# Kernel tuning notes

Measured on AMD Instinct MI355X. Metric: run time of the kernel, lower is better.

The kernel has to match this reference:

```python
import jax, jax.numpy as jnp
import numpy as np


def setup_inputs() -> dict:
    key = jax.random.key(0)
    ks = jax.random.split(key, 8)
    dim, E = 128, 8
    b, t, h, w = 2, 16, 64, 64
    scale = 1.0 / np.sqrt(dim)
    return {
        "x": jax.random.normal(ks[0], (b, dim, t, h, w), jnp.float32),
        "gate_w": jax.random.normal(ks[1], (dim, E), jnp.float32) * scale,
        "gate_b": jax.random.normal(ks[2], (E,), jnp.float32) * 0.01,
        "W1": jax.random.normal(ks[3], (E, dim, dim), jnp.float32) * scale,
        "b1": jax.random.normal(ks[4], (E, dim), jnp.float32) * 0.01,
        "alpha": jnp.full((E,), 0.25, jnp.float32),  # PReLU default init
        "W2": jax.random.normal(ks[5], (E, dim, dim), jnp.float32) * scale,
        "b2": jax.random.normal(ks[6], (E, dim), jnp.float32) * 0.01,
        "top_k": 2,
    }


def reference(x, gate_w, gate_b, W1, b1, alpha, W2, b2, top_k):
    b, c, t, h, w = x.shape
    E = gate_w.shape[1]
    # tokens: [N, c] with N = b*t*h*w (matches permute(0,2,3,4,1).reshape(-1,c))
    xf = jnp.transpose(x, (0, 2, 3, 4, 1)).reshape(-1, c)
    N = xf.shape[0]
    logits = xf @ gate_w + gate_b                      # [N, E]
    vals, idx = jax.lax.top_k(logits, top_k)           # [N, K]
    probs = jax.nn.softmax(vals, axis=1)               # softmax over selected logits
    # scatter combine weights to dense [N, E] (zero for unselected experts)
    combine = jnp.zeros((N, E), xf.dtype).at[jnp.arange(N)[:, None], idx].add(probs)
    # expert MLP (1x1x1 conv == per-token linear), scalar PReLU per expert
    h1 = jnp.einsum('nc,eoc->eno', xf, W1) + b1[:, None, :]          # [E, N, c]
    h1 = jnp.maximum(h1, 0) + alpha[:, None, None] * jnp.minimum(h1, 0)
    h2 = jnp.einsum('eno,epo->enp', h1, W2) + b2[:, None, :]         # [E, N, c]
    out = jnp.einsum('ne,enc->nc', combine, h2)                      # weighted combine
    out = jnp.transpose(out.reshape(b, t, h, w, c), (0, 4, 1, 2, 3))
    return out + x
```

## Files before the change

kernel.cpp:

```cpp
#include <hip/hip_runtime.h>

typedef float f32x4  __attribute__((ext_vector_type(4)));
typedef float f32x16 __attribute__((ext_vector_type(16)));
typedef __bf16 bf16x8 __attribute__((ext_vector_type(8)));

#define SPAT 65536
#define CH   128
#define NE   8

#define SLOTA   0
#define SLOTB   32768
#define GW_OFF  65536
#define B1_OFF  69632
#define B2T_OFF 73728
#define AL_OFF  77824
#define LDS_BYTES 77856

static __device__ __forceinline__ unsigned short f2b(float f) {
    unsigned u = __builtin_bit_cast(unsigned, f);
    unsigned r = u + 0x7FFFu + ((u >> 16) & 1u);
    return (unsigned short)(r >> 16);
}
static __device__ __forceinline__ unsigned pk2(float a, float b) {
    return (unsigned)f2b(a) | ((unsigned)f2b(b) << 16);
}

typedef const __attribute__((address_space(1))) void* as1cp;
typedef __attribute__((address_space(3))) void* as3p;
static __device__ __forceinline__ void gload16(const void* g, void* l) {
    __builtin_amdgcn_global_load_lds((as1cp)g, (as3p)l, 16, 0, 0);
}

__global__ void conv_w(const float* __restrict__ W1, const float* __restrict__ W2,
                       unsigned char* __restrict__ wimg) {
    const int gid = blockIdx.x * 256 + threadIdx.x;
    const int mat = gid >> 14;
    const int e   = (gid >> 11) & 7;
    const int r   = (gid >> 4) & 127;
    const int p   = gid & 15;
    const int sg  = p ^ (r & 15);
    int src_row = r;
    if (mat == 0) {
        const int n = 4 * (r >> 5) + ((r >> 3) & 3);
        src_row = (n >> 1) * 16 + ((r >> 2) & 1) * 8 + (n & 1) * 4 + (r & 3);
    }
    const float* s = (mat ? W2 : W1) + (e * 16384 + src_row * 128 + sg * 8);
    uint4 pk;
    pk.x = pk2(s[0], s[1]); pk.y = pk2(s[2], s[3]);
    pk.z = pk2(s[4], s[5]); pk.w = pk2(s[6], s[7]);
    *(uint4*)(wimg + mat * 262144 + e * 32768 + r * 256 + p * 16) = pk;
}

static __device__ __forceinline__ void stage_w(const unsigned char* __restrict__ src,
                                               unsigned char* dst, int t) {
    const int off = t * 16;
    gload16(src + off,          dst + off);
    gload16(src + 8192  + off,  dst + 8192  + off);
    gload16(src + 16384 + off,  dst + 16384 + off);
    gload16(src + 24576 + off,  dst + 24576 + off);
}

__global__ __launch_bounds__(512, 2)
void moe_main(const float* __restrict__ x,  const float* __restrict__ gw,
              const float* __restrict__ gb, const float* __restrict__ b1,
              const float* __restrict__ alpha, const float* __restrict__ b2,
              const unsigned char* __restrict__ wimg, float* __restrict__ out)
{
    __shared__ __align__(16) unsigned char smem[LDS_BYTES];
    const int t = threadIdx.x, lane = t & 63, w = t >> 6, blk = blockIdx.x;
    const int ltok = lane & 31, hi = lane >> 5, l15 = lane & 15;
    const size_t xbase = (size_t)(blk >> 8) * (size_t)(CH * SPAT) + (size_t)((blk & 255) << 8);
    const int m = w * 32 + ltok;

    stage_w(wimg,          smem + SLOTA, t);
    stage_w(wimg + 262144, smem + SLOTB, t);

    float v[8][8];
    #pragma unroll
    for (int kc = 0; kc < 8; ++kc)
        #pragma unroll
        for (int j = 0; j < 8; ++j)
            v[kc][j] = x[xbase + (size_t)(kc * 16 + hi * 8 + j) * SPAT + m];

    if (t < 256)      ((f32x4*)(smem + GW_OFF))[t]       = ((const f32x4*)gw)[t];
    else              ((f32x4*)(smem + B1_OFF))[t - 256] = ((const f32x4*)b1)[t - 256];
    if (t < 128) {
        uint4 pkv, z4 = {0u, 0u, 0u, 0u};
        pkv.x = pk2(b2[0 * 128 + t], b2[1 * 128 + t]);
        pkv.y = pk2(b2[2 * 128 + t], b2[3 * 128 + t]);
        pkv.z = pk2(b2[4 * 128 + t], b2[5 * 128 + t]);
        pkv.w = pk2(b2[6 * 128 + t], b2[7 * 128 + t]);
        *(uint4*)(smem + B2T_OFF + t * 32)      = pkv;
        *(uint4*)(smem + B2T_OFF + t * 32 + 16) = z4;
    } else if (t >= 128 && t < 136) {
        ((float*)(smem + AL_OFF))[t - 128] = alpha[t - 128];
    }
    __syncthreads();

    f32x4 plo = {0.f,0.f,0.f,0.f}, phi = {0.f,0.f,0.f,0.f};
    uint4 xb[8];
    #pragma unroll
    for (int kc = 0; kc < 8; ++kc) {
        const int c0 = kc * 16 + hi * 8;
        #pragma unroll
        for (int j = 0; j < 8; ++j) {
            const f32x4 g0 = *(const f32x4*)(smem + GW_OFF + (c0 + j) * 32);
            const f32x4 g1 = *(const f32x4*)(smem + GW_OFF + (c0 + j) * 32 + 16);
            plo += v[kc][j] * g0; phi += v[kc][j] * g1;
        }
        xb[kc].x = pk2(v[kc][0], v[kc][1]); xb[kc].y = pk2(v[kc][2], v[kc][3]);
        xb[kc].z = pk2(v[kc][4], v[kc][5]); xb[kc].w = pk2(v[kc][6], v[kc][7]);
    }
    #pragma unroll
    for (int i2 = 0; i2 < 4; ++i2) {
        plo[i2] += __shfl_xor(plo[i2], 32, 64);
        phi[i2] += __shfl_xor(phi[i2], 32, 64);
    }
    int i0, i1; float q0, q1; uint4 cbw;
    {
        float lg[8];
        #pragma unroll
        for (int e2 = 0; e2 < 4; ++e2) { lg[e2] = plo[e2] + gb[e2]; lg[4 + e2] = phi[e2] + gb[4 + e2]; }
        i0 = 0; float v0 = lg[0];
        #pragma unroll
        for (int e2 = 1; e2 < 8; ++e2) if (lg[e2] > v0) { v0 = lg[e2]; i0 = e2; }
        i1 = -1; float v1 = -3.4e38f;
        #pragma unroll
        for (int e2 = 0; e2 < 8; ++e2) if (e2 != i0 && lg[e2] > v1) { v1 = lg[e2]; i1 = e2; }
        const float d = expf(v1 - v0);
        q0 = 1.f / (1.f + d);
        q1 = d   / (1.f + d);
        float cb[8];
        #pragma unroll
        for (int e2 = 0; e2 < 8; ++e2) cb[e2] = (e2 == i0) ? q0 : ((e2 == i1) ? q1 : 0.f);
        cbw.x = pk2(cb[0], cb[1]); cbw.y = pk2(cb[2], cb[3]);
        cbw.z = pk2(cb[4], cb[5]); cbw.w = pk2(cb[6], cb[7]);
    }

    f32x16 acc[4] = {};

    #pragma unroll 1
    for (int e = 0; e < NE; ++e) {
        const float alph = ((const float*)(smem + AL_OFF))[e];
        const float ce = (i0 == e) ? q0 : ((i1 == e) ? q1 : 0.f);

        uint4 pa[8];
        #pragma unroll 2
        for (int g = 0; g < 4; ++g) {
            uint4 a1[8];
            #pragma unroll
            for (int kc = 0; kc < 8; ++kc)
                a1[kc] = *(const uint4*)(smem + SLOTA + (g * 32 + ltok) * 256
                                          + (((kc * 2 + hi) ^ l15) * 16));
            f32x16 h = {};
            #pragma unroll
            for (int kc = 0; kc < 8; ++kc)
                h = __builtin_amdgcn_mfma_f32_32x32x16_bf16(
                        __builtin_bit_cast(bf16x8, a1[kc]),
                        __builtin_bit_cast(bf16x8, xb[kc]), h, 0, 0, 0);
            #pragma unroll
            for (int q = 0; q < 4; ++q) {
                const int n = 4 * g + q, kt2 = n >> 1, half = q & 1;
                const int obase = kt2 * 16 + hi * 8 + half * 4;
                const f32x4 b1v = *(const f32x4*)(smem + B1_OFF + e * 512 + obase * 4);
                float hv[4];
                #pragma unroll
                for (int i = 0; i < 4; ++i) {
                    float z = h[q * 4 + i] + b1v[i];
                    z = (z > 0.f) ? z : alph * z;
                    hv[i] = z * ce;
                }
                ((unsigned*)&pa[kt2])[half * 2]     = pk2(hv[0], hv[1]);
                ((unsigned*)&pa[kt2])[half * 2 + 1] = pk2(hv[2], hv[3]);
            }
        }
        __syncthreads();
        if (e < 7) stage_w(wimg + (e + 1) * 32768, smem + SLOTA, t);

        #pragma unroll
        for (int kt2 = 0; kt2 < 8; ++kt2) {
            uint4 wf[4];
            #pragma unroll
            for (int n2 = 0; n2 < 4; ++n2)
                wf[n2] = *(const uint4*)(smem + SLOTB + (n2 * 32 + ltok) * 256
                                          + (((kt2 * 2 + hi) ^ l15) * 16));
            #pragma unroll
            for (int n2 = 0; n2 < 4; ++n2)
                acc[n2] = __builtin_amdgcn_mfma_f32_32x32x16_bf16(
                        __builtin_bit_cast(bf16x8, pa[kt2]),
                        __builtin_bit_cast(bf16x8, wf[n2]), acc[n2], 0, 0, 0);
        }
        if (e < 7) {
            __syncthreads();
            stage_w(wimg + 262144 + (e + 1) * 32768, smem + SLOTB, t);
        }
    }

    {
        const uint4 z4 = {0u, 0u, 0u, 0u};
        const uint4 aop = hi ? z4 : cbw;
        #pragma unroll
        for (int n2 = 0; n2 < 4; ++n2) {
            const uint4 bop = *(const uint4*)(smem + B2T_OFF + (n2 * 32 + ltok) * 32 + hi * 16);
            acc[n2] = __builtin_amdgcn_mfma_f32_32x32x16_bf16(
                    __builtin_bit_cast(bf16x8, aop),
                    __builtin_bit_cast(bf16x8, bop), acc[n2], 0, 0, 0);
        }
    }

    #pragma unroll
    for (int n2 = 0; n2 < 4; ++n2) {
        const int p = n2 * 32 + ltok;
        #pragma unroll
        for (int q = 0; q < 4; ++q) {
            const int tok0 = w * 32 + q * 8 + hi * 4;
            const size_t a = xbase + (size_t)p * SPAT + tok0;
            const f32x4 xv = *(const f32x4*)(x + a);
            f32x4 r;
            #pragma unroll
            for (int i = 0; i < 4; ++i) r[i] = acc[n2][q * 4 + i] + xv[i];
            *(f32x4*)(out + a) = r;
        }
    }
}

extern "C" void kernel_launch(void* const* d_in, const int* in_sizes, int n_in,
                              void* d_out, int out_size, void* d_ws, size_t ws_size,
                              hipStream_t stream) {
    const float* x  = (const float*)d_in[0];
    const float* gw = (const float*)d_in[1];
    const float* gb = (const float*)d_in[2];
    const float* W1 = (const float*)d_in[3];
    const float* b1 = (const float*)d_in[4];
    const float* al = (const float*)d_in[5];
    const float* W2 = (const float*)d_in[6];
    const float* b2 = (const float*)d_in[7];
    (void)in_sizes; (void)n_in; (void)out_size; (void)ws_size;
    unsigned char* wimg = (unsigned char*)d_ws;
    float* out = (float*)d_out;

    conv_w<<<dim3(128), dim3(256), 0, stream>>>(W1, W2, wimg);
    moe_main<<<dim3(512), dim3(512), 0, stream>>>(x, gw, gb, b1, al, b2, wimg, out);
}
```

Baseline: 148.9 us.

## Double-buffer expert weights in LDS and fuse second GEMM into chunk loop

Expands LDS to four 32KB weight slots so the next expert's W1 and W2 tiles are prefetched at the top of each iteration while the current pair is consumed. This cuts the barriers per expert from two to one. The second GEMM is interleaved per 32-row chunk of the first, so only two packed activation fragments stay live instead of eight. Gate weights are now read straight from global memory, and x is loaded per channel chunk rather than all up front. The cost is that LDS use grows to about 139KB per block, which likely allows only one 512-thread block per CU instead of two, lowering occupancy and latency hiding.

```diff
diff --git a/kernel.cpp b/kernel.cpp
--- a/kernel.cpp
+++ b/kernel.cpp
@@ -8,13 +8,11 @@
 #define CH   128
 #define NE   8
 
-#define SLOTA   0
-#define SLOTB   32768
-#define GW_OFF  65536
-#define B1_OFF  69632
-#define B2T_OFF 73728
-#define AL_OFF  77824
-#define LDS_BYTES 77856
+#define SLOT(i)  ((i) * 32768)
+#define B1_OFF   131072
+#define B2T_OFF  135168
+#define AL_OFF   139264
+#define LDS_BYTES 139296
 
 static __device__ __forceinline__ unsigned short f2b(float f) {
     unsigned u = __builtin_bit_cast(unsigned, f);
@@ -60,7 +58,7 @@
     gload16(src + 24576 + off,  dst + 24576 + off);
 }
 
-__global__ __launch_bounds__(512, 2)
+__global__ __launch_bounds__(512) __attribute__((amdgpu_waves_per_eu(2, 2)))
 void moe_main(const float* __restrict__ x,  const float* __restrict__ gw,
               const float* __restrict__ gb, const float* __restrict__ b1,
               const float* __restrict__ alpha, const float* __restrict__ b2,
@@ -72,18 +70,10 @@
     const size_t xbase = (size_t)(blk >> 8) * (size_t)(CH * SPAT) + (size_t)((blk & 255) << 8);
     const int m = w * 32 + ltok;
 
-    stage_w(wimg,          smem + SLOTA, t);
-    stage_w(wimg + 262144, smem + SLOTB, t);
-
-    float v[8][8];
-    #pragma unroll
-    for (int kc = 0; kc < 8; ++kc)
-        #pragma unroll
-        for (int j = 0; j < 8; ++j)
-            v[kc][j] = x[xbase + (size_t)(kc * 16 + hi * 8 + j) * SPAT + m];
-
-    if (t < 256)      ((f32x4*)(smem + GW_OFF))[t]       = ((const f32x4*)gw)[t];
-    else              ((f32x4*)(smem + B1_OFF))[t - 256] = ((const f32x4*)b1)[t - 256];
+    stage_w(wimg,          smem + SLOT(0), t);
+    stage_w(wimg + 262144, smem + SLOT(1), t);
+
+    if (t < 256) ((f32x4*)(smem + B1_OFF))[t] = ((const f32x4*)b1)[t];
     if (t < 128) {
         uint4 pkv, z4 = {0u, 0u, 0u, 0u};
         pkv.x = pk2(b2[0 * 128 + t], b2[1 * 128 + t]);
@@ -95,21 +85,23 @@
     } else if (t >= 128 && t < 136) {
         ((float*)(smem + AL_OFF))[t - 128] = alpha[t - 128];
     }
-    __syncthreads();
 
     f32x4 plo = {0.f,0.f,0.f,0.f}, phi = {0.f,0.f,0.f,0.f};
     uint4 xb[8];
     #pragma unroll
     for (int kc = 0; kc < 8; ++kc) {
         const int c0 = kc * 16 + hi * 8;
+        float v8[8];
+        #pragma unroll
+        for (int j = 0; j < 8; ++j) v8[j] = x[xbase + (size_t)(c0 + j) * SPAT + m];
         #pragma unroll
         for (int j = 0; j < 8; ++j) {
-            const f32x4 g0 = *(const f32x4*)(smem + GW_OFF + (c0 + j) * 32);
-            const f32x4 g1 = *(const f32x4*)(smem + GW_OFF + (c0 + j) * 32 + 16);
-            plo += v[kc][j] * g0; phi += v[kc][j] * g1;
-        }
-        xb[kc].x = pk2(v[kc][0], v[kc][1]); xb[kc].y = pk2(v[kc][2], v[kc][3]);
-        xb[kc].z = pk2(v[kc][4], v[kc][5]); xb[kc].w = pk2(v[kc][6], v[kc][7]);
+            const f32x4 g0 = *(const f32x4*)(gw + (c0 + j) * NE);
+            const f32x4 g1 = *(const f32x4*)(gw + (c0 + j) * NE + 4);
+            plo += v8[j] * g0; phi += v8[j] * g1;
+        }
+        xb[kc].x = pk2(v8[0], v8[1]); xb[kc].y = pk2(v8[2], v8[3]);
+        xb[kc].z = pk2(v8[4], v8[5]); xb[kc].w = pk2(v8[6], v8[7]);
     }
     #pragma unroll
     for (int i2 = 0; i2 < 4; ++i2) {
@@ -136,21 +128,28 @@
         cbw.x = pk2(cb[0], cb[1]); cbw.y = pk2(cb[2], cb[3]);
         cbw.z = pk2(cb[4], cb[5]); cbw.w = pk2(cb[6], cb[7]);
     }
+    __syncthreads();
 
     f32x16 acc[4] = {};
 
     #pragma unroll 1
     for (int e = 0; e < NE; ++e) {
+        const int cur = (e & 1) << 1;
+        if (e < 7) {
+            stage_w(wimg + (e + 1) * 32768,          smem + SLOT(cur ^ 2), t);
+            stage_w(wimg + 262144 + (e + 1) * 32768, smem + SLOT((cur ^ 2) + 1), t);
+        }
+        const unsigned char* WA = smem + SLOT(cur);
+        const unsigned char* WB = smem + SLOT(cur) + 32768;
         const float alph = ((const float*)(smem + AL_OFF))[e];
         const float ce = (i0 == e) ? q0 : ((i1 == e) ? q1 : 0.f);
 
-        uint4 pa[8];
-        #pragma unroll 2
+        #pragma unroll 1
         for (int g = 0; g < 4; ++g) {
             uint4 a1[8];
             #pragma unroll
             for (int kc = 0; kc < 8; ++kc)
-                a1[kc] = *(const uint4*)(smem + SLOTA + (g * 32 + ltok) * 256
+                a1[kc] = *(const uint4*)(WA + (g * 32 + ltok) * 256
                                           + (((kc * 2 + hi) ^ l15) * 16));
             f32x16 h = {};
             #pragma unroll
@@ -158,9 +157,10 @@
                 h = __builtin_amdgcn_mfma_f32_32x32x16_bf16(
                         __builtin_bit_cast(bf16x8, a1[kc]),
                         __builtin_bit_cast(bf16x8, xb[kc]), h, 0, 0, 0);
+            uint4 pa2[2];
             #pragma unroll
             for (int q = 0; q < 4; ++q) {
-                const int n = 4 * g + q, kt2 = n >> 1, half = q & 1;
+                const int n = 4 * g + q, kt2 = n >> 1, half = n & 1;
                 const int obase = kt2 * 16 + hi * 8 + half * 4;
                 const f32x4 b1v = *(const f32x4*)(smem + B1_OFF + e * 512 + obase * 4);
                 float hv[4];
@@ -170,30 +170,23 @@
                     z = (z > 0.f) ? z : alph * z;
                     hv[i] = z * ce;
                 }
-                ((unsigned*)&pa[kt2])[half * 2]     = pk2(hv[0], hv[1]);
-                ((unsigned*)&pa[kt2])[half * 2 + 1] = pk2(hv[2], hv[3]);
+                ((unsigned*)&pa2[q >> 1])[half * 2]     = pk2(hv[0], hv[1]);
+                ((unsigned*)&pa2[q >> 1])[half * 2 + 1] = pk2(hv[2], hv[3]);
             }
+            #pragma unroll
+            for (int dk = 0; dk < 2; ++dk) {
+                const int kt2 = 2 * g + dk;
+                #pragma unroll
+                for (int n2 = 0; n2 < 4; ++n2) {
+                    const uint4 wf = *(const uint4*)(WB + (n2 * 32 + ltok) * 256
+                                          + (((kt2 * 2 + hi) ^ l15) * 16));
+                    acc[n2] = __builtin_amdgcn_mfma_f32_32x32x16_bf16(
+                            __builtin_bit_cast(bf16x8, pa2[dk]),
+                            __builtin_bit_cast(bf16x8, wf), acc[n2], 0, 0, 0);
+                }
+            }
         }
         __syncthreads();
-        if (e < 7) stage_w(wimg + (e + 1) * 32768, smem + SLOTA, t);
-
-        #pragma unroll
-        for (int kt2 = 0; kt2 < 8; ++kt2) {
-            uint4 wf[4];
-            #pragma unroll
-            for (int n2 = 0; n2 < 4; ++n2)
-                wf[n2] = *(const uint4*)(smem + SLOTB + (n2 * 32 + ltok) * 256
-                                          + (((kt2 * 2 + hi) ^ l15) * 16));
-            #pragma unroll
-            for (int n2 = 0; n2 < 4; ++n2)
-                acc[n2] = __builtin_amdgcn_mfma_f32_32x32x16_bf16(
-                        __builtin_bit_cast(bf16x8, pa[kt2]),
-                        __builtin_bit_cast(bf16x8, wf[n2]), acc[n2], 0, 0, 0);
-        }
-        if (e < 7) {
-            __syncthreads();
-            stage_w(wimg + 262144 + (e + 1) * 32768, smem + SLOTB, t);
-        }
     }
 
     {
```

Result: faster. 121.0 us (-18.7%).
